# Optimization experiments

Measured on AMD Instinct MI355X. Metric: run time of the kernel, lower is better.

The kernel has to match this reference:

```python
import jax, jax.numpy as jnp
import numpy as np

DF = 2  # downsampling_factor

def _conv1x1(x, w, b):
    # x: [N,C,T,H,W], w: [O,C], b: [O]
    return jnp.einsum('ncthw,oc->nothw', x, w) + b[None, :, None, None, None]

def _avgpool(x):
    # AvgPool3d(kernel=(1,k,k), stride=(1,s,s), pad=(0,p,p)), count_include_pad=True
    k, s = DF + 1, DF
    p = (DF + 1) // 2
    summed = jax.lax.reduce_window(
        x, 0.0, jax.lax.add,
        window_dimensions=(1, 1, 1, k, k),
        window_strides=(1, 1, 1, s, s),
        padding=((0, 0), (0, 0), (0, 0), (p, p), (p, p)))
    return summed / float(k * k)

def _grid(T, Hd, Wd, t_scale):
    xg = jnp.arange(Wd, dtype=jnp.float32) / ((Wd - 1) * 0.25) - 2.0
    yg = jnp.arange(Hd, dtype=jnp.float32) / ((Hd - 1) * 0.5) - 1.0
    tg = (jnp.arange(T, dtype=jnp.float32) / ((T - 1) * 0.5) - 1.0) * t_scale
    return jnp.stack(jnp.meshgrid(tg, yg, xg, indexing='ij'), axis=0)  # [3,T,Hd,Wd]

def setup_inputs() -> dict:
    key = jax.random.key(0)
    ks = jax.random.split(key, 9)
    C, IC, OC = 256, 128, 256
    x = jax.random.normal(ks[0], (2, C, 4, 64, 64), dtype=jnp.float32)
    sc = 0.05
    return {
        'x': x,
        'theta_w': jax.random.normal(ks[1], (IC, C), jnp.float32) * sc,
        'theta_b': jax.random.normal(ks[2], (IC,), jnp.float32) * sc,
        'phi_w': jax.random.normal(ks[3], (IC, C), jnp.float32) * sc,
        'phi_b': jax.random.normal(ks[4], (IC,), jnp.float32) * sc,
        'g_w': jax.random.normal(ks[5], (IC, C), jnp.float32) * sc,
        'g_b': jax.random.normal(ks[6], (IC,), jnp.float32) * sc,
        'W_w': jax.random.normal(ks[7], (OC, IC + 3), jnp.float32) * sc,
        'W_b': jax.random.normal(ks[8], (OC,), jnp.float32) * sc,
    }

def reference(x, theta_w, theta_b, phi_w, phi_b, g_w, g_b, W_w, W_b):
    N, C, T, H, W = x.shape
    IC = theta_w.shape[0]
    theta_x = _conv1x1(x, theta_w, theta_b)                       # [N,IC,T,H,W]
    theta_x = theta_x.transpose(0, 2, 3, 4, 1).reshape(N, T * H * W, IC)
    phi_x = _avgpool(_conv1x1(x, phi_w, phi_b))                   # [N,IC,T,Hd,Wd]
    Hd, Wd = phi_x.shape[-2], phi_x.shape[-1]
    phi_x = phi_x.reshape(N, IC, T * Hd * Wd)
    f_x = jax.nn.softmax(jnp.matmul(theta_x, phi_x), axis=-1)     # [N,THW,THdWd]
    g_x = _avgpool(_conv1x1(x, g_w, g_b))                         # [N,IC,T,Hd,Wd]
    grid = _grid(T, Hd, Wd, 0.1)                                   # [3,T,Hd,Wd]
    g_x = jnp.concatenate(
        [g_x, jnp.broadcast_to(grid[None], (N, 3, T, Hd, Wd))], axis=1)
    g_x = g_x.transpose(0, 2, 3, 4, 1).reshape(N, T * Hd * Wd, IC + 3)
    y = jnp.matmul(f_x, g_x)                                       # [N,THW,IC+3]
    y = y.transpose(0, 2, 1).reshape(N, IC + 3, T, H, W)
    return _conv1x1(y, W_w, W_b)
```

## Files before the change

kernel.cpp:

```cpp
#include <hip/hip_runtime.h>
#include <stdint.h>

typedef short short8 __attribute__((ext_vector_type(8)));
typedef float floatx4 __attribute__((ext_vector_type(4)));
typedef float floatx16 __attribute__((ext_vector_type(16)));
typedef unsigned uint4v __attribute__((ext_vector_type(4)));

#define MFMA16(a, b, c) __builtin_amdgcn_mfma_f32_16x16x32_bf16((a), (b), (c), 0, 0, 0)
#define MFMA32(a, b, c) __builtin_amdgcn_mfma_f32_32x32x16_bf16((a), (b), (c), 0, 0, 0)

#define SPLITS 3

__device__ __forceinline__ unsigned short f2bf(float f) {
    union { float f; unsigned u; } v; v.f = f;
    unsigned u = v.u;
    unsigned r = (u + 0x7FFFu + ((u >> 16) & 1u)) >> 16;
    return (unsigned short)r;
}
__device__ __forceinline__ unsigned pkfast(float lo, float hi) {
    unsigned a = __float_as_uint(lo) + 0x8000u;
    unsigned b = __float_as_uint(hi) + 0x8000u;
    return __builtin_amdgcn_perm(b, a, 0x07060302u);
}

__global__ void k_prep(const float* th, const float* ph, const float* gw, const float* Ww,
                       unsigned short* TW, unsigned short* PW, unsigned short* GW,
                       unsigned short* Wp) {
    int i = blockIdx.x * 256 + threadIdx.x;
    if (i < 32768) {
        TW[i] = f2bf(th[i]);
    } else if (i < 65536) {
        PW[i - 32768] = f2bf(ph[i - 32768]);
    } else if (i < 98304) {
        GW[i - 65536] = f2bf(gw[i - 65536]);
    } else if (i < 98304 + 256 * 160) {
        int j = i - 98304;
        int oc = j / 160, k = j - oc * 160;
        Wp[j] = (k < 131) ? f2bf(Ww[oc * 131 + k]) : (unsigned short)0;
    }
}

__global__ void k_pool(const float* __restrict__ x, float* __restrict__ xp) {
    int e = blockIdx.x * 256 + threadIdx.x;
    int wd = e & 31, hd = (e >> 5) & 31, t = (e >> 10) & 3, c = (e >> 12) & 255, n = e >> 20;
    const float* base = x + (((size_t)(n * 256 + c) * 4 + t) << 12);
    int h0 = 2 * hd - 1, w0 = 2 * wd - 1;
    float s = 0.f;
    #pragma unroll
    for (int dh = 0; dh < 3; ++dh) {
        int h = h0 + dh;
        if ((unsigned)h < 64u) {
            const float* row = base + h * 64;
            #pragma unroll
            for (int dw = 0; dw < 3; ++dw) {
                int w = w0 + dw;
                if ((unsigned)w < 64u) s += row[w];
            }
        }
    }
    xp[((size_t)(n * 256 + c) << 12) + (t << 10) + (hd << 5) + wd] = s * (1.f / 9.f);
}

__launch_bounds__(256)
__global__ void k_convq(const float* __restrict__ x, const unsigned short* __restrict__ TW,
                        const float* __restrict__ tb, unsigned short* __restrict__ Q) {
    __shared__ unsigned short Qs[4][16][132];
    int tid = threadIdx.x, wid = tid >> 6, lane = tid & 63, quad = lane >> 4, l16 = lane & 15;
    int n = blockIdx.y;
    int px0 = blockIdx.x * 64 + wid * 16;
    const float* xb = x + ((size_t)n << 22) + px0 + l16;
    floatx4 acc[8];
    #pragma unroll
    for (int i = 0; i < 8; ++i) acc[i] = (floatx4)0.f;
    for (int kc = 0; kc < 8; ++kc) {
        int cbase = kc * 32 + quad * 8;
        uint4v bu;
        #pragma unroll
        for (int j = 0; j < 4; ++j)
            bu[j] = pkfast(xb[(size_t)(cbase + 2 * j) << 14],
                           xb[(size_t)(cbase + 2 * j + 1) << 14]);
        short8 b = __builtin_bit_cast(short8, bu);
        #pragma unroll
        for (int mt = 0; mt < 8; ++mt) {
            short8 a = *(const short8*)(TW + (mt * 16 + l16) * 256 + cbase);
            acc[mt] = MFMA16(a, b, acc[mt]);
        }
    }
    #pragma unroll
    for (int mt = 0; mt < 8; ++mt) {
        int ic = mt * 16 + quad * 4;
        uint2 w;
        w.x = pkfast(acc[mt][0] + tb[ic], acc[mt][1] + tb[ic + 1]);
        w.y = pkfast(acc[mt][2] + tb[ic + 2], acc[mt][3] + tb[ic + 3]);
        *(uint2*)&Qs[wid][l16][ic] = w;
    }
    #pragma unroll
    for (int i = 0; i < 4; ++i) {
        int pxl = i * 4 + quad;
        short8 row = *(const short8*)&Qs[wid][pxl][l16 * 8];
        *(short8*)(Q + ((((size_t)n << 14) + px0 + pxl) << 7) + l16 * 8) = row;
    }
}

__launch_bounds__(256)
__global__ void k_convkv(const float* __restrict__ xp,
                         const unsigned short* __restrict__ PW, const float* __restrict__ pb,
                         const unsigned short* __restrict__ GW, const float* __restrict__ gb,
                         unsigned short* __restrict__ K, unsigned short* __restrict__ Vt) {
    __shared__ unsigned short Sh[8576];
    int tid = threadIdx.x, wid = tid >> 6, lane = tid & 63, quad = lane >> 4, l16 = lane & 15;
    int n = blockIdx.y;
    int k0 = blockIdx.x * 64;
    int key = k0 + wid * 16 + l16;
    const float* xb = xp + ((size_t)n << 20) + key;
    floatx4 ka[8], va[8];
    #pragma unroll
    for (int i = 0; i < 8; ++i) { ka[i] = (floatx4)0.f; va[i] = (floatx4)0.f; }
    for (int kc = 0; kc < 8; ++kc) {
        int cbase = kc * 32 + quad * 8;
        uint4v bu;
        #pragma unroll
        for (int j = 0; j < 4; ++j)
            bu[j] = pkfast(xb[(size_t)(cbase + 2 * j) << 12],
                           xb[(size_t)(cbase + 2 * j + 1) << 12]);
        short8 b = __builtin_bit_cast(short8, bu);
        #pragma unroll
        for (int mt = 0; mt < 8; ++mt) {
            short8 ap = *(const short8*)(PW + (mt * 16 + l16) * 256 + cbase);
            ka[mt] = MFMA16(ap, b, ka[mt]);
            short8 ag = *(const short8*)(GW + (mt * 16 + l16) * 256 + cbase);
            va[mt] = MFMA16(ag, b, va[mt]);
        }
    }
    int hd = (key >> 5) & 31, wdd = key & 31;
    float frac = ((hd == 0) ? 2.f : 3.f) * ((wdd == 0) ? 2.f : 3.f) * (1.f / 9.f);

    unsigned short (*Ks)[132] = (unsigned short(*)[132])(Sh + wid * 2112);
    #pragma unroll
    for (int mt = 0; mt < 8; ++mt) {
        int ic = mt * 16 + quad * 4;
        uint2 w;
        w.x = pkfast(ka[mt][0] + pb[ic] * frac, ka[mt][1] + pb[ic + 1] * frac);
        w.y = pkfast(ka[mt][2] + pb[ic + 2] * frac, ka[mt][3] + pb[ic + 3] * frac);
        *(uint2*)&Ks[l16][ic] = w;
    }
    #pragma unroll
    for (int i = 0; i < 4; ++i) {
        int pxl = i * 4 + quad;
        short8 row = *(const short8*)&Ks[pxl][l16 * 8];
        *(short8*)(K + ((((size_t)n << 12) + k0 + wid * 16 + pxl) << 7) + l16 * 8) = row;
    }

    __syncthreads();
    unsigned short (*Vs)[134] = (unsigned short(*)[134])Sh;
    #pragma unroll
    for (int mt = 0; mt < 8; ++mt) {
        int ic = mt * 16 + quad * 4;
        uint2 w;
        w.x = pkfast(va[mt][0] + gb[ic] * frac, va[mt][1] + gb[ic + 1] * frac);
        w.y = pkfast(va[mt][2] + gb[ic + 2] * frac, va[mt][3] + gb[ic + 3] * frac);
        *(uint2*)&Vs[wid * 16 + l16][ic] = w;
    }
    __syncthreads();
    #pragma unroll
    for (int it2 = 0; it2 < 4; ++it2) {
        int ic = it2 * 32 + (tid >> 3);
        int kk = (tid & 7) * 8;
        uint4v w;
        #pragma unroll
        for (int j = 0; j < 4; ++j) {
            unsigned s0 = Vs[kk + 2 * j][ic];
            unsigned s1 = Vs[kk + 2 * j + 1][ic];
            w[j] = s0 | (s1 << 16);
        }
        *(uint4v*)(Vt + (((size_t)(n * 160 + ic)) << 12) + k0 + kk) = w;
    }

    #pragma unroll
    for (int it = 0; it < 8; ++it) {
        int e = it * 256 + tid;
        int row = 128 + (e >> 6);
        int kk = k0 + (e & 63);
        int t = kk >> 10, hh = (kk >> 5) & 31, ww = kk & 31;
        unsigned short v = 0;
        if (row == 128) v = f2bf(((float)t * (1.f / 1.5f) - 1.f) * 0.1f);
        else if (row == 129) v = f2bf((float)hh * (1.f / 15.5f) - 1.f);
        else if (row == 130) v = f2bf((float)ww * (1.f / 7.75f) - 2.f);
        Vt[(((size_t)n * 160 + row) << 12) + kk] = v;
    }
}

__launch_bounds__(256, 3)
__global__ void k_attn(const unsigned short* __restrict__ Q, const unsigned short* __restrict__ K,
                       const unsigned short* __restrict__ Vt, unsigned short* __restrict__ Y,
                       float* __restrict__ L) {
    __shared__ short Klds[64][136];
    __shared__ short Vlds[160][72];
    int tid = threadIdx.x, wid = tid >> 6, lane = tid & 63;
    int l32 = lane & 31, half = lane >> 5;
    int n = blockIdx.y, sp = blockIdx.z;
    int c0 = (sp * 64) / SPLITS, c1 = ((sp + 1) * 64) / SPLITS;
    int nch = c1 - c0;
    int q0 = blockIdx.x * 128 + wid * 32;

    const unsigned short* Qr = Q + ((((size_t)n << 14) + q0 + l32) << 7);
    short8 qf[8];
    #pragma unroll
    for (int kc = 0; kc < 8; ++kc) qf[kc] = *(const short8*)(Qr + kc * 16 + half * 8);

    floatx16 O[5];
    #pragma unroll
    for (int t = 0; t < 5; ++t) O[t] = (floatx16)0.f;
    float lacc = 0.f;

    int krow = tid >> 4, kcol = (tid & 15) * 8;
    int vrow = tid >> 3, vcol = (tid & 7) * 8;
    const unsigned short* kptr = K + ((((size_t)n << 12) + c0 * 64 + krow) << 7) + kcol;
    const unsigned short* vptr = Vt + ((size_t)(n * 160 + vrow) << 12) + c0 * 64 + vcol;

    short8 kpre[4], vpre[5];
    #pragma unroll
    for (int i = 0; i < 4; ++i) kpre[i] = *(const short8*)(kptr + (size_t)i * 16 * 128);
    #pragma unroll
    for (int i = 0; i < 5; ++i) vpre[i] = *(const short8*)(vptr + ((size_t)i * 32 << 12));

    for (int it = 0; it < nch; ++it) {
        __syncthreads();
        #pragma unroll
        for (int i = 0; i < 4; ++i) *(short8*)&Klds[i * 16 + krow][kcol] = kpre[i];
        #pragma unroll
        for (int i = 0; i < 5; ++i) *(short8*)&Vlds[i * 32 + vrow][vcol] = vpre[i];
        __syncthreads();
        if (it + 1 < nch) {
            const unsigned short* kp = kptr + (size_t)(it + 1) * 64 * 128;
            const unsigned short* vp = vptr + (size_t)(it + 1) * 64;
            #pragma unroll
            for (int i = 0; i < 4; ++i) kpre[i] = *(const short8*)(kp + (size_t)i * 16 * 128);
            #pragma unroll
            for (int i = 0; i < 5; ++i) vpre[i] = *(const short8*)(vp + ((size_t)i * 32 << 12));
        }

        #pragma unroll
        for (int ks = 0; ks < 2; ++ks) {
            floatx16 st = (floatx16)0.f;
            #pragma unroll
            for (int kc = 0; kc < 8; ++kc) {
                short8 kf = *(const short8*)&Klds[ks * 32 + l32][kc * 16 + half * 8];
                st = MFMA32(kf, qf[kc], st);
            }
            unsigned u[8];
            #pragma unroll
            for (int a = 0; a < 4; ++a) {
                float p0 = exp2f(fmaf(st[4 * a + 0], 1.44269504f, -17.3123404907f));
                float p1 = exp2f(fmaf(st[4 * a + 1], 1.44269504f, -17.3123404907f));
                float p2 = exp2f(fmaf(st[4 * a + 2], 1.44269504f, -17.3123404907f));
                float p3 = exp2f(fmaf(st[4 * a + 3], 1.44269504f, -17.3123404907f));
                lacc += (p0 + p1) + (p2 + p3);
                u[2 * a] = pkfast(p0, p1);
                u[2 * a + 1] = pkfast(p2, p3);
            }
            unsigned xu[8];
            #pragma unroll
            for (int g = 0; g < 8; ++g) xu[g] = (unsigned)__shfl_xor((int)u[g], 32);
            uint4v pw0, pw1;
            pw0[0] = half ? xu[2] : u[0];
            pw0[1] = half ? xu[3] : u[1];
            pw0[2] = half ? u[2] : xu[0];
            pw0[3] = half ? u[3] : xu[1];
            pw1[0] = half ? xu[6] : u[4];
            pw1[1] = half ? xu[7] : u[5];
            pw1[2] = half ? u[6] : xu[4];
            pw1[3] = half ? u[7] : xu[5];
            short8 pf0 = __builtin_bit_cast(short8, pw0);
            short8 pf1 = __builtin_bit_cast(short8, pw1);
            #pragma unroll
            for (int vt = 0; vt < 5; ++vt) {
                short8 vf0 = *(const short8*)&Vlds[vt * 32 + l32][ks * 32 + half * 8];
                O[vt] = MFMA32(vf0, pf0, O[vt]);
                short8 vf1 = *(const short8*)&Vlds[vt * 32 + l32][ks * 32 + 16 + half * 8];
                O[vt] = MFMA32(vf1, pf1, O[vt]);
            }
        }
    }
    float lt = lacc + __shfl_xor(lacc, 32);
    int slab = sp * 2 + n;
    unsigned short* Yb = Y + ((((size_t)slab << 14) + q0 + l32) * 160);
    #pragma unroll
    for (int vt = 0; vt < 5; ++vt)
        #pragma unroll
        for (int g = 0; g < 4; ++g) {
            int vd = vt * 32 + 8 * g + 4 * half;
            uint2 w;
            w.x = pkfast(O[vt][4 * g], O[vt][4 * g + 1]);
            w.y = pkfast(O[vt][4 * g + 2], O[vt][4 * g + 3]);
            *(uint2*)(Yb + vd) = w;
        }
    if (lane < 32) L[(((size_t)slab) << 14) + q0 + lane] = lt;
}

__launch_bounds__(256)
__global__ void k_convf(const unsigned short* __restrict__ Y, const float* __restrict__ L,
                        const unsigned short* __restrict__ Wp, const float* __restrict__ Wb,
                        float* __restrict__ out) {
    int tid = threadIdx.x, wid = tid >> 6, lane = tid & 63, quad = lane >> 4, l16 = lane & 15;
    int n = blockIdx.y;
    int p0 = blockIdx.x * 64;
    floatx4 acc[4][4];
    #pragma unroll
    for (int i = 0; i < 4; ++i)
        #pragma unroll
        for (int j = 0; j < 4; ++j) acc[i][j] = (floatx4)0.f;
    for (int kc = 0; kc < 5; ++kc) {
        int cb = kc * 32 + quad * 8;
        short8 a[4];
        #pragma unroll
        for (int mt = 0; mt < 4; ++mt)
            a[mt] = *(const short8*)(Wp + (size_t)(wid * 64 + mt * 16 + l16) * 160 + cb);
        #pragma unroll
        for (int sp = 0; sp < SPLITS; ++sp) {
            const unsigned short* Yb = Y + ((((size_t)(sp * 2 + n)) << 14) + p0) * 160;
            #pragma unroll
            for (int nt = 0; nt < 4; ++nt) {
                short8 b = *(const short8*)(Yb + (size_t)(nt * 16 + l16) * 160 + cb);
                #pragma unroll
                for (int mt = 0; mt < 4; ++mt) acc[mt][nt] = MFMA16(a[mt], b, acc[mt][nt]);
            }
        }
    }
    float linv[4];
    #pragma unroll
    for (int nt = 0; nt < 4; ++nt) {
        int p = p0 + nt * 16 + l16;
        float ls = 0.f;
        #pragma unroll
        for (int sp = 0; sp < SPLITS; ++sp) ls += L[(((size_t)(sp * 2 + n)) << 14) + p];
        linv[nt] = 1.f / ls;
    }
    #pragma unroll
    for (int mt = 0; mt < 4; ++mt)
        #pragma unroll
        for (int r = 0; r < 4; ++r) {
            int oc = wid * 64 + mt * 16 + quad * 4 + r;
            float bb = Wb[oc];
            float* orow = out + ((((size_t)n << 8) + oc) << 14) + p0;
            #pragma unroll
            for (int nt = 0; nt < 4; ++nt)
                orow[nt * 16 + l16] = acc[mt][nt][r] * linv[nt] + bb;
        }
}

extern "C" void kernel_launch(void* const* d_in, const int* in_sizes, int n_in,
                              void* d_out, int out_size, void* d_ws, size_t ws_size,
                              hipStream_t stream) {
    (void)in_sizes; (void)n_in; (void)out_size; (void)ws_size;
    const float* x   = (const float*)d_in[0];
    const float* thw = (const float*)d_in[1];
    const float* thb = (const float*)d_in[2];
    const float* phw = (const float*)d_in[3];
    const float* phb = (const float*)d_in[4];
    const float* gw_ = (const float*)d_in[5];
    const float* gb_ = (const float*)d_in[6];
    const float* Ww  = (const float*)d_in[7];
    const float* Wb  = (const float*)d_in[8];
    float* out = (float*)d_out;

    char* ws = (char*)d_ws;
    size_t off = 0;
    auto alloc = [&](size_t b) { size_t o = off; off += (b + 255) & ~(size_t)255; return o; };
    unsigned short* TW = (unsigned short*)(ws + alloc(32768 * 2));
    unsigned short* PW = (unsigned short*)(ws + alloc(32768 * 2));
    unsigned short* GW = (unsigned short*)(ws + alloc(32768 * 2));
    unsigned short* Wp = (unsigned short*)(ws + alloc(40960 * 2));
    unsigned short* Qb = (unsigned short*)(ws + alloc((size_t)32768 * 128 * 2));
    unsigned short* Kb = (unsigned short*)(ws + alloc((size_t)8192 * 128 * 2));
    unsigned short* Vt = (unsigned short*)(ws + alloc((size_t)2 * 160 * 4096 * 2));
    float*          Lb = (float*)(ws + alloc((size_t)SPLITS * 2 * 16384 * 4));
    size_t ybytes = (size_t)SPLITS * 2 * 16384 * 160 * 2;
    unsigned short* Yb = (unsigned short*)(ws + alloc(ybytes));
    float*          xp = (float*)((char*)Yb + (ybytes - (size_t)2 * 256 * 4096 * 4));

    k_prep<<<(139264 + 255) / 256, 256, 0, stream>>>(thw, phw, gw_, Ww, TW, PW, GW, Wp);
    k_pool<<<8192, 256, 0, stream>>>(x, xp);
    k_convq<<<dim3(256, 2), 256, 0, stream>>>(x, TW, thb, Qb);
    k_convkv<<<dim3(64, 2), 256, 0, stream>>>(xp, PW, phb, GW, gb_, Kb, Vt);
    k_attn<<<dim3(128, 2, SPLITS), 256, 0, stream>>>(Qb, Kb, Vt, Yb, Lb);
    k_convf<<<dim3(256, 2), 256, 0, stream>>>(Yb, Lb, Wp, Wb, out);
}
```

Before: 309.4 us.

## Stage K/V in padded chunk layout and load via global_load_lds

k_convkv now writes K and V^T into a per-chunk staging buffer that already has the padded LDS layout (row strides of 136 and 72). k_attn then copies each 40 KB chunk straight into shared memory with global_load_lds, skipping the register round-trip and ds_write. The price is the register prefetch of the next chunk: each iteration now issues its loads and waits on vmcnt(0) before computing, so load latency is no longer overlapped with compute except through other resident blocks. The softmax/PV body is moved into a helper function.

```diff
diff --git a/kernel.cpp b/kernel.cpp
--- a/kernel.cpp
+++ b/kernel.cpp
@@ -10,6 +10,16 @@
 #define MFMA32(a, b, c) __builtin_amdgcn_mfma_f32_32x32x16_bf16((a), (b), (c), 0, 0, 0)
 
 #define SPLITS 3
+#define CHUNK_BYTES 40960
+#define CHUNK_SHORTS 20480
+#define VOFF_SHORTS 8704
+
+typedef __attribute__((address_space(1))) const void* gas1_cp;
+typedef __attribute__((address_space(3))) void* las3_p;
+
+__device__ __forceinline__ void gload_lds16(const void* g, void* l) {
+    __builtin_amdgcn_global_load_lds((gas1_cp)g, (las3_p)l, 16, 0, 0);
+}
 
 __device__ __forceinline__ unsigned short f2bf(float f) {
     union { float f; unsigned u; } v; v.f = f;
@@ -106,12 +116,14 @@
 __global__ void k_convkv(const float* __restrict__ xp,
                          const unsigned short* __restrict__ PW, const float* __restrict__ pb,
                          const unsigned short* __restrict__ GW, const float* __restrict__ gb,
-                         unsigned short* __restrict__ K, unsigned short* __restrict__ Vt) {
+                         unsigned short* __restrict__ Stg) {
     __shared__ unsigned short Sh[8576];
     int tid = threadIdx.x, wid = tid >> 6, lane = tid & 63, quad = lane >> 4, l16 = lane & 15;
     int n = blockIdx.y;
-    int k0 = blockIdx.x * 64;
+    int chunk = blockIdx.x;
+    int k0 = chunk * 64;
     int key = k0 + wid * 16 + l16;
+    unsigned short* sc = Stg + (size_t)(n * 64 + chunk) * CHUNK_SHORTS;
     const float* xb = xp + ((size_t)n << 20) + key;
     floatx4 ka[8], va[8];
     #pragma unroll
@@ -148,7 +160,7 @@
     for (int i = 0; i < 4; ++i) {
         int pxl = i * 4 + quad;
         short8 row = *(const short8*)&Ks[pxl][l16 * 8];
-        *(short8*)(K + ((((size_t)n << 12) + k0 + wid * 16 + pxl) << 7) + l16 * 8) = row;
+        *(short8*)(sc + (wid * 16 + pxl) * 136 + l16 * 8) = row;
     }
 
     __syncthreads();
@@ -173,29 +185,66 @@
             unsigned s1 = Vs[kk + 2 * j + 1][ic];
             w[j] = s0 | (s1 << 16);
         }
-        *(uint4v*)(Vt + (((size_t)(n * 160 + ic)) << 12) + k0 + kk) = w;
+        *(uint4v*)(sc + VOFF_SHORTS + ic * 72 + kk) = w;
     }
 
     #pragma unroll
     for (int it = 0; it < 8; ++it) {
         int e = it * 256 + tid;
         int row = 128 + (e >> 6);
-        int kk = k0 + (e & 63);
+        int kl = e & 63;
+        int kk = k0 + kl;
         int t = kk >> 10, hh = (kk >> 5) & 31, ww = kk & 31;
         unsigned short v = 0;
         if (row == 128) v = f2bf(((float)t * (1.f / 1.5f) - 1.f) * 0.1f);
         else if (row == 129) v = f2bf((float)hh * (1.f / 15.5f) - 1.f);
         else if (row == 130) v = f2bf((float)ww * (1.f / 7.75f) - 2.f);
-        Vt[(((size_t)n * 160 + row) << 12) + kk] = v;
+        sc[VOFF_SHORTS + row * 72 + kl] = v;
+    }
+}
+
+__device__ __forceinline__ void softmax_pv(const floatx16 st, int ks,
+                                           const short (*Vlds)[72], floatx16* O,
+                                           float& lacc, int l32, int half) {
+    unsigned u[8];
+    #pragma unroll
+    for (int a = 0; a < 4; ++a) {
+        float p0 = exp2f(fmaf(st[4 * a + 0], 1.44269504f, -17.3123404907f));
+        float p1 = exp2f(fmaf(st[4 * a + 1], 1.44269504f, -17.3123404907f));
+        float p2 = exp2f(fmaf(st[4 * a + 2], 1.44269504f, -17.3123404907f));
+        float p3 = exp2f(fmaf(st[4 * a + 3], 1.44269504f, -17.3123404907f));
+        lacc += (p0 + p1) + (p2 + p3);
+        u[2 * a] = pkfast(p0, p1);
+        u[2 * a + 1] = pkfast(p2, p3);
+    }
+    unsigned xu[8];
+    #pragma unroll
+    for (int g = 0; g < 8; ++g) xu[g] = (unsigned)__shfl_xor((int)u[g], 32);
+    uint4v pw0, pw1;
+    pw0[0] = half ? xu[2] : u[0];
+    pw0[1] = half ? xu[3] : u[1];
+    pw0[2] = half ? u[2] : xu[0];
+    pw0[3] = half ? u[3] : xu[1];
+    pw1[0] = half ? xu[6] : u[4];
+    pw1[1] = half ? xu[7] : u[5];
+    pw1[2] = half ? u[6] : xu[4];
+    pw1[3] = half ? u[7] : xu[5];
+    short8 pf0 = __builtin_bit_cast(short8, pw0);
+    short8 pf1 = __builtin_bit_cast(short8, pw1);
+    #pragma unroll
+    for (int vt = 0; vt < 5; ++vt) {
+        short8 vf0 = *(const short8*)&Vlds[vt * 32 + l32][ks * 32 + half * 8];
+        O[vt] = MFMA32(vf0, pf0, O[vt]);
+        short8 vf1 = *(const short8*)&Vlds[vt * 32 + l32][ks * 32 + 16 + half * 8];
+        O[vt] = MFMA32(vf1, pf1, O[vt]);
     }
 }
 
 __launch_bounds__(256, 3)
-__global__ void k_attn(const unsigned short* __restrict__ Q, const unsigned short* __restrict__ K,
-                       const unsigned short* __restrict__ Vt, unsigned short* __restrict__ Y,
-                       float* __restrict__ L) {
-    __shared__ short Klds[64][136];
-    __shared__ short Vlds[160][72];
+__global__ void k_attn(const unsigned short* __restrict__ Q,
+                       const unsigned char* __restrict__ Stg,
+                       unsigned short* __restrict__ Y, float* __restrict__ L) {
+    __shared__ __align__(16) char Sh[CHUNK_BYTES];
     int tid = threadIdx.x, wid = tid >> 6, lane = tid & 63;
     int l32 = lane & 31, half = lane >> 5;
     int n = blockIdx.y, sp = blockIdx.z;
@@ -213,32 +262,21 @@
     for (int t = 0; t < 5; ++t) O[t] = (floatx16)0.f;
     float lacc = 0.f;
 
-    int krow = tid >> 4, kcol = (tid & 15) * 8;
-    int vrow = tid >> 3, vcol = (tid & 7) * 8;
-    const unsigned short* kptr = K + ((((size_t)n << 12) + c0 * 64 + krow) << 7) + kcol;
-    const unsigned short* vptr = Vt + ((size_t)(n * 160 + vrow) << 12) + c0 * 64 + vcol;
-
-    short8 kpre[4], vpre[5];
-    #pragma unroll
-    for (int i = 0; i < 4; ++i) kpre[i] = *(const short8*)(kptr + (size_t)i * 16 * 128);
-    #pragma unroll
-    for (int i = 0; i < 5; ++i) vpre[i] = *(const short8*)(vptr + ((size_t)i * 32 << 12));
+    const short (*Klds)[136] = (const short(*)[136])Sh;
+    const short (*Vlds)[72] = (const short(*)[72])(Sh + 17408);
+
+    const unsigned char* gsl = Stg + ((size_t)(n * 64 + c0)) * CHUNK_BYTES
+                               + (wid * 10) * 1024 + lane * 16;
+    char* lsl = Sh + (wid * 10) * 1024;
 
     for (int it = 0; it < nch; ++it) {
         __syncthreads();
-        #pragma unroll
-        for (int i = 0; i < 4; ++i) *(short8*)&Klds[i * 16 + krow][kcol] = kpre[i];
-        #pragma unroll
-        for (int i = 0; i < 5; ++i) *(short8*)&Vlds[i * 32 + vrow][vcol] = vpre[i];
+        const unsigned char* g = gsl + (size_t)it * CHUNK_BYTES;
+        #pragma unroll
+        for (int i = 0; i < 10; ++i)
+            gload_lds16(g + i * 1024, lsl + i * 1024);
+        asm volatile("s_waitcnt vmcnt(0)" ::: "memory");
         __syncthreads();
-        if (it + 1 < nch) {
-            const unsigned short* kp = kptr + (size_t)(it + 1) * 64 * 128;
-            const unsigned short* vp = vptr + (size_t)(it + 1) * 64;
-            #pragma unroll
-            for (int i = 0; i < 4; ++i) kpre[i] = *(const short8*)(kp + (size_t)i * 16 * 128);
-            #pragma unroll
-            for (int i = 0; i < 5; ++i) vpre[i] = *(const short8*)(vp + ((size_t)i * 32 << 12));
-        }
 
         #pragma unroll
         for (int ks = 0; ks < 2; ++ks) {
@@ -248,38 +286,7 @@
                 short8 kf = *(const short8*)&Klds[ks * 32 + l32][kc * 16 + half * 8];
                 st = MFMA32(kf, qf[kc], st);
             }
-            unsigned u[8];
-            #pragma unroll
-            for (int a = 0; a < 4; ++a) {
-                float p0 = exp2f(fmaf(st[4 * a + 0], 1.44269504f, -17.3123404907f));
-                float p1 = exp2f(fmaf(st[4 * a + 1], 1.44269504f, -17.3123404907f));
-                float p2 = exp2f(fmaf(st[4 * a + 2], 1.44269504f, -17.3123404907f));
-                float p3 = exp2f(fmaf(st[4 * a + 3], 1.44269504f, -17.3123404907f));
-                lacc += (p0 + p1) + (p2 + p3);
-                u[2 * a] = pkfast(p0, p1);
-                u[2 * a + 1] = pkfast(p2, p3);
-            }
-            unsigned xu[8];
-            #pragma unroll
-            for (int g = 0; g < 8; ++g) xu[g] = (unsigned)__shfl_xor((int)u[g], 32);
-            uint4v pw0, pw1;
-            pw0[0] = half ? xu[2] : u[0];
-            pw0[1] = half ? xu[3] : u[1];
-            pw0[2] = half ? u[2] : xu[0];
-            pw0[3] = half ? u[3] : xu[1];
-            pw1[0] = half ? xu[6] : u[4];
-            pw1[1] = half ? xu[7] : u[5];
-            pw1[2] = half ? u[6] : xu[4];
-            pw1[3] = half ? u[7] : xu[5];
-            short8 pf0 = __builtin_bit_cast(short8, pw0);
-            short8 pf1 = __builtin_bit_cast(short8, pw1);
-            #pragma unroll
-            for (int vt = 0; vt < 5; ++vt) {
-                short8 vf0 = *(const short8*)&Vlds[vt * 32 + l32][ks * 32 + half * 8];
-                O[vt] = MFMA32(vf0, pf0, O[vt]);
-                short8 vf1 = *(const short8*)&Vlds[vt * 32 + l32][ks * 32 + 16 + half * 8];
-                O[vt] = MFMA32(vf1, pf1, O[vt]);
-            }
+            softmax_pv(st, ks, Vlds, O, lacc, l32, half);
         }
     }
     float lt = lacc + __shfl_xor(lacc, 32);
@@ -372,8 +379,7 @@
     unsigned short* GW = (unsigned short*)(ws + alloc(32768 * 2));
     unsigned short* Wp = (unsigned short*)(ws + alloc(40960 * 2));
     unsigned short* Qb = (unsigned short*)(ws + alloc((size_t)32768 * 128 * 2));
-    unsigned short* Kb = (unsigned short*)(ws + alloc((size_t)8192 * 128 * 2));
-    unsigned short* Vt = (unsigned short*)(ws + alloc((size_t)2 * 160 * 4096 * 2));
+    unsigned short* St = (unsigned short*)(ws + alloc((size_t)2 * 64 * CHUNK_BYTES));
     float*          Lb = (float*)(ws + alloc((size_t)SPLITS * 2 * 16384 * 4));
     size_t ybytes = (size_t)SPLITS * 2 * 16384 * 160 * 2;
     unsigned short* Yb = (unsigned short*)(ws + alloc(ybytes));
@@ -382,7 +388,7 @@
     k_prep<<<(139264 + 255) / 256, 256, 0, stream>>>(thw, phw, gw_, Ww, TW, PW, GW, Wp);
     k_pool<<<8192, 256, 0, stream>>>(x, xp);
     k_convq<<<dim3(256, 2), 256, 0, stream>>>(x, TW, thb, Qb);
-    k_convkv<<<dim3(64, 2), 256, 0, stream>>>(xp, PW, phb, GW, gb_, Kb, Vt);
-    k_attn<<<dim3(128, 2, SPLITS), 256, 0, stream>>>(Qb, Kb, Vt, Yb, Lb);
+    k_convkv<<<dim3(64, 2), 256, 0, stream>>>(xp, PW, phb, GW, gb_, St);
+    k_attn<<<dim3(128, 2, SPLITS), 256, 0, stream>>>(Qb, (const unsigned char*)St, Yb, Lb);
     k_convf<<<dim3(256, 2), 256, 0, stream>>>(Yb, Lb, Wp, Wb, out);
 }
```

Measured after the change: 274.6 us. 11.2% less time.
